# Optimization experiments

Measured on AMD Instinct MI355X. Metric: run time of the kernel, lower is better.

Reference implementation:

```python
import jax, jax.numpy as jnp
import numpy as np

N_EMBDS = 1024
N_HEADS = 16
HEAD_DIM = N_EMBDS // N_HEADS


def setup_inputs() -> dict:
    key = jax.random.key(0)
    ks = jax.random.split(key, 5)
    B, T, C = 2, 2048, N_EMBDS
    x = jax.random.normal(ks[0], (B, T, C), dtype=jnp.float32)
    s = 1.0 / np.sqrt(C)
    W_attn = jax.random.normal(ks[1], (C, 3 * C), dtype=jnp.float32) * s
    b_attn = jnp.zeros((3 * C,), dtype=jnp.float32)
    W_proj = jax.random.normal(ks[2], (C, C), dtype=jnp.float32) * s
    b_proj = jnp.zeros((C,), dtype=jnp.float32)
    return {"x": x, "W_attn": W_attn, "b_attn": b_attn, "W_proj": W_proj, "b_proj": b_proj}


def reference(x, W_attn, b_attn, W_proj, b_proj):
    B, T, C = x.shape
    H, D = N_HEADS, HEAD_DIM
    qkv = x @ W_attn + b_attn  # [B, T, 3C]
    q, k, v = jnp.split(qkv, 3, axis=-1)
    # [B, H, T, D]
    q = q.reshape(B, T, H, D).transpose(0, 2, 1, 3)
    k = k.reshape(B, T, H, D).transpose(0, 2, 1, 3)
    v = v.reshape(B, T, H, D).transpose(0, 2, 1, 3)
    att = jnp.einsum('bhqd,bhkd->bhqk', q, k) * (1.0 / np.sqrt(D))  # [B,H,T,T]
    causal = jnp.tril(jnp.ones((T, T), dtype=bool))
    att = jnp.where(causal[None, None], att, -jnp.inf)
    att = jax.nn.softmax(att, axis=-1)
    y = jnp.einsum('bhqk,bhkd->bhqd', att, v)  # [B,H,T,D]
    y = y.transpose(0, 2, 1, 3).reshape(B, T, C)
    return y @ W_proj + b_proj
```

## Files before the change

kernel.cpp:

```cpp
#include <hip/hip_runtime.h>
#include <hip/hip_bf16.h>


typedef __bf16 bf16x8 __attribute__((ext_vector_type(8)));
typedef float  f32x4  __attribute__((ext_vector_type(4)));
#define BF16 __hip_bfloat16

constexpr int Bb = 2, Tt = 2048, Cc = 1024, Hh = 16, Dd = 64;
constexpr float NEG_INF = -1e30f;

__device__ __forceinline__ f32x4 mfma16(bf16x8 a, bf16x8 b, f32x4 c) {
  return __builtin_amdgcn_mfma_f32_16x16x32_bf16(a, b, c, 0, 0, 0);
}

__device__ __forceinline__ void gll16(const void* g, void* l) {
  __builtin_amdgcn_global_load_lds((const __attribute__((address_space(1))) void*)g,
                                   (__attribute__((address_space(3))) void*)l,
                                   16, 0, 0);
}

__device__ __forceinline__ int swz64(int r, int c) {
  return r * 64 + ((((c >> 3) ^ r) & 7) << 3) + (c & 7);
}

__global__ void cast_kernel(const float* __restrict__ in, BF16* __restrict__ out,
                            int n) {
  const int i = (blockIdx.x * 256 + threadIdx.x) * 8;
  const float4 a = *(const float4*)&in[i];
  const float4 b = *(const float4*)&in[i + 4];
  BF16 o[8];
  o[0] = __float2bfloat16(a.x); o[1] = __float2bfloat16(a.y);
  o[2] = __float2bfloat16(a.z); o[3] = __float2bfloat16(a.w);
  o[4] = __float2bfloat16(b.x); o[5] = __float2bfloat16(b.y);
  o[6] = __float2bfloat16(b.z); o[7] = __float2bfloat16(b.w);
  *(uint4*)&out[i] = *(const uint4*)o;
}

__global__ void transpose_cast(const float* __restrict__ in, BF16* __restrict__ outT,
                               int K, int N) {
  __shared__ float tile[32][33];
  const int n0 = blockIdx.x * 32, k0 = blockIdx.y * 32;
  const int tx = threadIdx.x, ty = threadIdx.y;
#pragma unroll
  for (int i = ty; i < 32; i += 8) tile[i][tx] = in[(size_t)(k0 + i) * N + (n0 + tx)];
  __syncthreads();
#pragma unroll
  for (int i = ty; i < 32; i += 8)
    outT[(size_t)(n0 + i) * K + (k0 + tx)] = __float2bfloat16(tile[tx][i]);
}

__global__ void transpose_v(const BF16* __restrict__ in, BF16* __restrict__ out) {
  __shared__ BF16 tile[32][33];
  const int t0 = blockIdx.x * 32, d0 = blockIdx.y * 32, bh = blockIdx.z;
  const BF16* src = in + (size_t)bh * Tt * Dd;
  BF16* dst = out + (size_t)bh * Tt * Dd;
  const int tx = threadIdx.x, ty = threadIdx.y;
#pragma unroll
  for (int i = ty; i < 32; i += 8) tile[i][tx] = src[(size_t)(t0 + i) * Dd + (d0 + tx)];
  __syncthreads();
#pragma unroll
  for (int i = ty; i < 32; i += 8) dst[(size_t)(d0 + i) * Tt + (t0 + tx)] = tile[tx][i];
}

template <int MODE>
__global__ __launch_bounds__(256) void gemm_bt(const BF16* __restrict__ A,
                                               const BF16* __restrict__ Bt,
                                               const float* __restrict__ bias,
                                               BF16* __restrict__ oq,
                                               BF16* __restrict__ ok,
                                               BF16* __restrict__ ov,
                                               float* __restrict__ fout,
                                               int Ndim, int Kdim) {
  __shared__ alignas(16) BF16 sA[128 * 32];
  __shared__ alignas(16) BF16 sB[128 * 32];
  const int tid = threadIdx.x;
  const int wave = tid >> 6, lane = tid & 63;
  const int quad = lane >> 4, l16 = lane & 15;
  const int wm = (wave >> 1) * 64, wn = (wave & 1) * 64;
  const int bm = blockIdx.y * 128, bn = blockIdx.x * 128;

  f32x4 acc[4][4];
#pragma unroll
  for (int i = 0; i < 4; ++i)
#pragma unroll
    for (int j = 0; j < 4; ++j) acc[i][j] = f32x4{0.f, 0.f, 0.f, 0.f};

  const int rowA = wave * 32 + (lane >> 2);
  const int sub8 = (lane & 3) * 8;
  const BF16* gA0 = &A[(size_t)(bm + rowA) * Kdim + sub8];
  const BF16* gB0 = &Bt[(size_t)(bn + rowA) * Kdim + sub8];
  const size_t rstep16 = (size_t)16 * Kdim;
  BF16* lA0 = &sA[wave * 1024];
  BF16* lA1 = &sA[wave * 1024 + 512];
  BF16* lB0 = &sB[wave * 1024];
  BF16* lB1 = &sB[wave * 1024 + 512];

  for (int k0 = 0; k0 < Kdim; k0 += 32) {
    __syncthreads();
    gll16(gA0 + k0, lA0);
    gll16(gA0 + rstep16 + k0, lA1);
    gll16(gB0 + k0, lB0);
    gll16(gB0 + rstep16 + k0, lB1);
    __syncthreads();

    bf16x8 af[4], bf_[4];
#pragma unroll
    for (int i = 0; i < 4; ++i)
      af[i] = *(const bf16x8*)&sA[(wm + i * 16 + l16) * 32 + quad * 8];
#pragma unroll
    for (int j = 0; j < 4; ++j)
      bf_[j] = *(const bf16x8*)&sB[(wn + j * 16 + l16) * 32 + quad * 8];
#pragma unroll
    for (int i = 0; i < 4; ++i)
#pragma unroll
      for (int j = 0; j < 4; ++j) acc[i][j] = mfma16(af[i], bf_[j], acc[i][j]);
  }

#pragma unroll
  for (int j = 0; j < 4; ++j) {
    const int gn = bn + wn + j * 16 + l16;
    const float bsv = bias[gn];
#pragma unroll
    for (int i = 0; i < 4; ++i) {
#pragma unroll
      for (int r = 0; r < 4; ++r) {
        const int gm = bm + wm + i * 16 + quad * 4 + r;
        float val = acc[i][j][r] + bsv;
        if (MODE == 0) {
          const int which = gn >> 10, c = gn & 1023;
          const int hh = c >> 6, dd = c & 63;
          const int bb = gm >> 11, tk = gm & 2047;
          if (which == 0) val *= 0.125f;
          BF16* dst = (which == 0) ? oq : (which == 1) ? ok : ov;
          dst[(((size_t)(bb * Hh + hh)) * Tt + tk) * Dd + dd] = __float2bfloat16(val);
        } else {
          fout[(size_t)gm * Ndim + gn] = val;
        }
      }
    }
  }
}

__global__ __launch_bounds__(256) void attn_kernel(const BF16* __restrict__ qg,
                                                   const BF16* __restrict__ kg,
                                                   const BF16* __restrict__ vtg,
                                                   BF16* __restrict__ yb) {
  __shared__ alignas(16) BF16 sK[64 * 64];
  __shared__ alignas(16) BF16 sV[64 * 64];
  __shared__ alignas(16) BF16 sP[4][16 * 64];
  const int pr = blockIdx.x, h = blockIdx.y, b = blockIdx.z;
  const int qtA = pr, qtB = 31 - pr;
  const int tid = threadIdx.x;
  const int wave = tid >> 6, lane = tid & 63;
  const int quad = lane >> 4, l16 = lane & 15;
  const size_t base = ((size_t)(b * Hh + h)) * Tt * Dd;

  bf16x8 qA0, qA1, qB0, qB1;
  {
    const size_t offA = base + (size_t)(qtA * 64 + wave * 16 + l16) * Dd;
    const size_t offB = base + (size_t)(qtB * 64 + wave * 16 + l16) * Dd;
    qA0 = *(const bf16x8*)&qg[offA + quad * 8];
    qA1 = *(const bf16x8*)&qg[offA + 32 + quad * 8];
    qB0 = *(const bf16x8*)&qg[offB + quad * 8];
    qB1 = *(const bf16x8*)&qg[offB + 32 + quad * 8];
  }

  bf16x8 vones;
#pragma unroll
  for (int j = 0; j < 8; ++j) vones[j] = (__bf16)1.0f;

  f32x4 oA[4], oB[4], oLA, oLB;
#pragma unroll
  for (int i = 0; i < 4; ++i) {
    oA[i] = f32x4{0.f, 0.f, 0.f, 0.f};
    oB[i] = f32x4{0.f, 0.f, 0.f, 0.f};
  }
  oLA = f32x4{0.f, 0.f, 0.f, 0.f};
  oLB = f32x4{0.f, 0.f, 0.f, 0.f};

  const int krow = tid >> 2, kcg = (tid & 3) * 16;
  BF16* pw = &sP[wave][0];

  auto process = [&](int jt, int qt, bf16x8 qf0, bf16x8 qf1, f32x4 (&o)[4],
                     f32x4& oL) {
    const int kb = jt * 64;
    f32x4 s4[4];
#pragma unroll
    for (int t = 0; t < 4; ++t) s4[t] = f32x4{0.f, 0.f, 0.f, 0.f};
#pragma unroll
    for (int t = 0; t < 4; ++t) {
      const bf16x8 kf0 = *(const bf16x8*)&sK[swz64(t * 16 + l16, quad * 8)];
      const bf16x8 kf1 = *(const bf16x8*)&sK[swz64(t * 16 + l16, 32 + quad * 8)];
      s4[t] = mfma16(qf0, kf0, s4[t]);
      s4[t] = mfma16(qf1, kf1, s4[t]);
    }

    if (jt == qt) {
      const int qrow = qt * 64 + wave * 16 + quad * 4;
#pragma unroll
      for (int t = 0; t < 4; ++t)
#pragma unroll
        for (int r = 0; r < 4; ++r)
          if (kb + t * 16 + l16 > qrow + r) s4[t][r] = NEG_INF;
    }

#pragma unroll
    for (int t = 0; t < 4; ++t)
#pragma unroll
      for (int r = 0; r < 4; ++r) s4[t][r] = __expf(s4[t][r] - 12.0f);

    asm volatile("s_waitcnt lgkmcnt(0)" ::: "memory");
#pragma unroll
    for (int t = 0; t < 4; ++t)
#pragma unroll
      for (int r = 0; r < 4; ++r)
        pw[swz64(quad * 4 + r, t * 16 + l16)] = __float2bfloat16(s4[t][r]);
    asm volatile("s_waitcnt lgkmcnt(0)" ::: "memory");

#pragma unroll
    for (int c = 0; c < 2; ++c) {
      const bf16x8 pa = *(const bf16x8*)&pw[swz64(l16, c * 32 + quad * 8)];
#pragma unroll
      for (int dt = 0; dt < 4; ++dt) {
        const bf16x8 vb = *(const bf16x8*)&sV[swz64(dt * 16 + l16, c * 32 + quad * 8)];
        o[dt] = mfma16(pa, vb, o[dt]);
      }
      oL = mfma16(pa, vones, oL);
    }
  };

  for (int jt = 0; jt <= qtB; ++jt) {
    const int kb = jt * 64;
    __syncthreads();
    {
      const uint4* pk = (const uint4*)&kg[base + (size_t)(kb + krow) * Dd + kcg];
      const uint4* pv = (const uint4*)&vtg[base + (size_t)krow * Tt + kb + kcg];
      uint4 k0 = pk[0], k1 = pk[1];
      uint4 v0 = pv[0], v1 = pv[1];
      *(uint4*)&sK[swz64(krow, kcg)]     = k0;
      *(uint4*)&sK[swz64(krow, kcg + 8)] = k1;
      *(uint4*)&sV[swz64(krow, kcg)]     = v0;
      *(uint4*)&sV[swz64(krow, kcg + 8)] = v1;
    }
    __syncthreads();

    if (jt <= qtA) process(jt, qtA, qA0, qA1, oA, oLA);
    process(jt, qtB, qB0, qB1, oB, oLB);
  }

  auto epi = [&](int qt, f32x4 (&o)[4], f32x4& oL) {
#pragma unroll
    for (int r = 0; r < 4; ++r) {
      const float inv = 1.0f / oL[r];
      const int trow = qt * 64 + wave * 16 + quad * 4 + r;
#pragma unroll
      for (int dt = 0; dt < 4; ++dt)
        yb[((size_t)(b * Tt + trow)) * Cc + h * Dd + dt * 16 + l16] =
            __float2bfloat16(o[dt][r] * inv);
    }
  };
  epi(qtA, oA, oLA);
  epi(qtB, oB, oLB);
}

extern "C" void kernel_launch(void* const* d_in, const int* in_sizes, int n_in,
                              void* d_out, int out_size, void* d_ws, size_t ws_size,
                              hipStream_t stream) {
  (void)in_sizes; (void)n_in; (void)out_size; (void)ws_size;
  const float* x      = (const float*)d_in[0];
  const float* W_attn = (const float*)d_in[1];
  const float* b_attn = (const float*)d_in[2];
  const float* W_proj = (const float*)d_in[3];
  const float* b_proj = (const float*)d_in[4];
  float* out = (float*)d_out;

  constexpr size_t SZ_WA = (size_t)3072 * 1024;
  constexpr size_t SZ_WP = (size_t)1024 * 1024;
  constexpr size_t SZ_X  = (size_t)4096 * 1024;
  constexpr size_t SZ_T  = (size_t)Bb * Hh * Tt * Dd;

  BF16* ws   = (BF16*)d_ws;
  BF16* wtAb = ws;
  BF16* wtPb = wtAb + SZ_WA;
  BF16* xb   = wtPb + SZ_WP;
  BF16* q    = xb + SZ_X;
  BF16* k    = q + SZ_T;
  BF16* v    = k + SZ_T;
  BF16* vt   = v + SZ_T;
  BF16* yb   = vt + SZ_T;

  cast_kernel<<<dim3(2048), 256, 0, stream>>>(x, xb, (int)SZ_X);
  transpose_cast<<<dim3(96, 32), dim3(32, 8), 0, stream>>>(W_attn, wtAb, 1024, 3072);
  transpose_cast<<<dim3(32, 32), dim3(32, 8), 0, stream>>>(W_proj, wtPb, 1024, 1024);
  gemm_bt<0><<<dim3(24, 32), 256, 0, stream>>>(xb, wtAb, b_attn, q, k, v, nullptr,
                                               3072, 1024);
  transpose_v<<<dim3(64, 2, 32), dim3(32, 8), 0, stream>>>(v, vt);
  attn_kernel<<<dim3(16, 16, 2), 256, 0, stream>>>(q, k, vt, yb);
  gemm_bt<1><<<dim3(8, 32), 256, 0, stream>>>(yb, wtPb, b_proj, nullptr, nullptr,
                                              nullptr, out, 1024, 1024);
}
```

Baseline: 201.3 us.

## Keep softmax probabilities in registers via transposed S and fuse prep kernels

The attention kernel now computes S transposed (K as the A operand), so each lane's exp'd probabilities already form the A-fragment for a 16x16x16 bf16 MFMA against V. This removes the per-wave shared-memory round trip for P and its waitcnt barriers, and it interleaves the two query tiles so each K/V fragment read is shared by both. The three preprocessing launches (x cast, two weight transposes) are merged into one kernel indexed by block id to cut launch overhead. The trade-off is twice as many smaller-K MFMAs for PV, plus higher register pressure from holding both tiles' score accumulators at once.

```diff
diff --git a/kernel.cpp b/kernel.cpp
--- a/kernel.cpp
+++ b/kernel.cpp
@@ -3,6 +3,8 @@
 
 
 typedef __bf16 bf16x8 __attribute__((ext_vector_type(8)));
+typedef __bf16 bf16x4 __attribute__((ext_vector_type(4)));
+typedef short  short4v __attribute__((ext_vector_type(4)));
 typedef float  f32x4  __attribute__((ext_vector_type(4)));
 #define BF16 __hip_bfloat16
 
@@ -12,6 +14,23 @@
 __device__ __forceinline__ f32x4 mfma16(bf16x8 a, bf16x8 b, f32x4 c) {
   return __builtin_amdgcn_mfma_f32_16x16x32_bf16(a, b, c, 0, 0, 0);
 }
+
+#if __has_builtin(__builtin_amdgcn_mfma_f32_16x16x16bf16_1k)
+__device__ __forceinline__ f32x4 mfma16k(bf16x4 a, bf16x4 b, f32x4 c) {
+  return __builtin_amdgcn_mfma_f32_16x16x16bf16_1k(
+      __builtin_bit_cast(short4v, a), __builtin_bit_cast(short4v, b), c, 0, 0, 0);
+}
+#elif __has_builtin(__builtin_amdgcn_mfma_f32_16x16x16_bf16)
+__device__ __forceinline__ f32x4 mfma16k(bf16x4 a, bf16x4 b, f32x4 c) {
+  return __builtin_amdgcn_mfma_f32_16x16x16_bf16(a, b, c, 0, 0, 0);
+}
+#else
+__device__ __forceinline__ f32x4 mfma16k(bf16x4 a, bf16x4 b, f32x4 c) {
+  asm volatile("v_mfma_f32_16x16x16_bf16 %0, %1, %2, %0"
+               : "+v"(c) : "v"(a), "v"(b));
+  return c;
+}
+#endif
 
 __device__ __forceinline__ void gll16(const void* g, void* l) {
   __builtin_amdgcn_global_load_lds((const __attribute__((address_space(1))) void*)g,
@@ -23,24 +42,33 @@
   return r * 64 + ((((c >> 3) ^ r) & 7) << 3) + (c & 7);
 }
 
-__global__ void cast_kernel(const float* __restrict__ in, BF16* __restrict__ out,
-                            int n) {
-  const int i = (blockIdx.x * 256 + threadIdx.x) * 8;
-  const float4 a = *(const float4*)&in[i];
-  const float4 b = *(const float4*)&in[i + 4];
-  BF16 o[8];
-  o[0] = __float2bfloat16(a.x); o[1] = __float2bfloat16(a.y);
-  o[2] = __float2bfloat16(a.z); o[3] = __float2bfloat16(a.w);
-  o[4] = __float2bfloat16(b.x); o[5] = __float2bfloat16(b.y);
-  o[6] = __float2bfloat16(b.z); o[7] = __float2bfloat16(b.w);
-  *(uint4*)&out[i] = *(const uint4*)o;
-}
-
-__global__ void transpose_cast(const float* __restrict__ in, BF16* __restrict__ outT,
-                               int K, int N) {
+__global__ void prep_kernel(const float* __restrict__ x, BF16* __restrict__ xb,
+                            const float* __restrict__ Wa, BF16* __restrict__ WaT,
+                            const float* __restrict__ Wp, BF16* __restrict__ WpT) {
   __shared__ float tile[32][33];
-  const int n0 = blockIdx.x * 32, k0 = blockIdx.y * 32;
-  const int tx = threadIdx.x, ty = threadIdx.y;
+  const int bx = blockIdx.x, tid = threadIdx.x;
+  if (bx < 2048) {
+    const int i = (bx * 256 + tid) * 8;
+    const float4 a = *(const float4*)&x[i];
+    const float4 b = *(const float4*)&x[i + 4];
+    BF16 o[8];
+    o[0] = __float2bfloat16(a.x); o[1] = __float2bfloat16(a.y);
+    o[2] = __float2bfloat16(a.z); o[3] = __float2bfloat16(a.w);
+    o[4] = __float2bfloat16(b.x); o[5] = __float2bfloat16(b.y);
+    o[6] = __float2bfloat16(b.z); o[7] = __float2bfloat16(b.w);
+    *(uint4*)&xb[i] = *(const uint4*)o;
+    return;
+  }
+  const float* in; BF16* outT; int K, N, gx, gy;
+  if (bx < 5120) {
+    const int idx = bx - 2048;
+    in = Wa; outT = WaT; K = 1024; N = 3072; gx = idx % 96; gy = idx / 96;
+  } else {
+    const int idx = bx - 5120;
+    in = Wp; outT = WpT; K = 1024; N = 1024; gx = idx % 32; gy = idx / 32;
+  }
+  const int n0 = gx * 32, k0 = gy * 32;
+  const int tx = tid & 31, ty = tid >> 5;
 #pragma unroll
   for (int i = ty; i < 32; i += 8) tile[i][tx] = in[(size_t)(k0 + i) * N + (n0 + tx)];
   __syncthreads();
@@ -147,89 +175,36 @@
                                                    BF16* __restrict__ yb) {
   __shared__ alignas(16) BF16 sK[64 * 64];
   __shared__ alignas(16) BF16 sV[64 * 64];
-  __shared__ alignas(16) BF16 sP[4][16 * 64];
   const int pr = blockIdx.x, h = blockIdx.y, b = blockIdx.z;
-  const int qtA = pr, qtB = 31 - pr;
+  const int qt[2] = {pr, 31 - pr};
   const int tid = threadIdx.x;
   const int wave = tid >> 6, lane = tid & 63;
   const int quad = lane >> 4, l16 = lane & 15;
   const size_t base = ((size_t)(b * Hh + h)) * Tt * Dd;
 
-  bf16x8 qA0, qA1, qB0, qB1;
-  {
-    const size_t offA = base + (size_t)(qtA * 64 + wave * 16 + l16) * Dd;
-    const size_t offB = base + (size_t)(qtB * 64 + wave * 16 + l16) * Dd;
-    qA0 = *(const bf16x8*)&qg[offA + quad * 8];
-    qA1 = *(const bf16x8*)&qg[offA + 32 + quad * 8];
-    qB0 = *(const bf16x8*)&qg[offB + quad * 8];
-    qB1 = *(const bf16x8*)&qg[offB + 32 + quad * 8];
-  }
-
-  bf16x8 vones;
-#pragma unroll
-  for (int j = 0; j < 8; ++j) vones[j] = (__bf16)1.0f;
-
-  f32x4 oA[4], oB[4], oLA, oLB;
-#pragma unroll
-  for (int i = 0; i < 4; ++i) {
-    oA[i] = f32x4{0.f, 0.f, 0.f, 0.f};
-    oB[i] = f32x4{0.f, 0.f, 0.f, 0.f};
-  }
-  oLA = f32x4{0.f, 0.f, 0.f, 0.f};
-  oLB = f32x4{0.f, 0.f, 0.f, 0.f};
+  bf16x8 qf[2][2];
+#pragma unroll
+  for (int s = 0; s < 2; ++s) {
+    const size_t off = base + (size_t)(qt[s] * 64 + wave * 16 + l16) * Dd;
+    qf[s][0] = *(const bf16x8*)&qg[off + quad * 8];
+    qf[s][1] = *(const bf16x8*)&qg[off + 32 + quad * 8];
+  }
+
+  bf16x4 ones4;
+#pragma unroll
+  for (int j = 0; j < 4; ++j) ones4[j] = (__bf16)1.0f;
+
+  f32x4 o[2][4], oL[2];
+#pragma unroll
+  for (int s = 0; s < 2; ++s) {
+#pragma unroll
+    for (int i = 0; i < 4; ++i) o[s][i] = f32x4{0.f, 0.f, 0.f, 0.f};
+    oL[s] = f32x4{0.f, 0.f, 0.f, 0.f};
+  }
 
   const int krow = tid >> 2, kcg = (tid & 3) * 16;
-  BF16* pw = &sP[wave][0];
-
-  auto process = [&](int jt, int qt, bf16x8 qf0, bf16x8 qf1, f32x4 (&o)[4],
-                     f32x4& oL) {
-    const int kb = jt * 64;
-    f32x4 s4[4];
-#pragma unroll
-    for (int t = 0; t < 4; ++t) s4[t] = f32x4{0.f, 0.f, 0.f, 0.f};
-#pragma unroll
-    for (int t = 0; t < 4; ++t) {
-      const bf16x8 kf0 = *(const bf16x8*)&sK[swz64(t * 16 + l16, quad * 8)];
-      const bf16x8 kf1 = *(const bf16x8*)&sK[swz64(t * 16 + l16, 32 + quad * 8)];
-      s4[t] = mfma16(qf0, kf0, s4[t]);
-      s4[t] = mfma16(qf1, kf1, s4[t]);
-    }
-
-    if (jt == qt) {
-      const int qrow = qt * 64 + wave * 16 + quad * 4;
-#pragma unroll
-      for (int t = 0; t < 4; ++t)
-#pragma unroll
-        for (int r = 0; r < 4; ++r)
-          if (kb + t * 16 + l16 > qrow + r) s4[t][r] = NEG_INF;
-    }
-
-#pragma unroll
-    for (int t = 0; t < 4; ++t)
-#pragma unroll
-      for (int r = 0; r < 4; ++r) s4[t][r] = __expf(s4[t][r] - 12.0f);
-
-    asm volatile("s_waitcnt lgkmcnt(0)" ::: "memory");
-#pragma unroll
-    for (int t = 0; t < 4; ++t)
-#pragma unroll
-      for (int r = 0; r < 4; ++r)
-        pw[swz64(quad * 4 + r, t * 16 + l16)] = __float2bfloat16(s4[t][r]);
-    asm volatile("s_waitcnt lgkmcnt(0)" ::: "memory");
-
-#pragma unroll
-    for (int c = 0; c < 2; ++c) {
-      const bf16x8 pa = *(const bf16x8*)&pw[swz64(l16, c * 32 + quad * 8)];
-#pragma unroll
-      for (int dt = 0; dt < 4; ++dt) {
-        const bf16x8 vb = *(const bf16x8*)&sV[swz64(dt * 16 + l16, c * 32 + quad * 8)];
-        o[dt] = mfma16(pa, vb, o[dt]);
-      }
-      oL = mfma16(pa, vones, oL);
-    }
-  };
-
-  for (int jt = 0; jt <= qtB; ++jt) {
+
+  for (int jt = 0; jt <= qt[1]; ++jt) {
     const int kb = jt * 64;
     __syncthreads();
     {
@@ -244,23 +219,66 @@
     }
     __syncthreads();
 
-    if (jt <= qtA) process(jt, qtA, qA0, qA1, oA, oLA);
-    process(jt, qtB, qB0, qB1, oB, oLB);
-  }
-
-  auto epi = [&](int qt, f32x4 (&o)[4], f32x4& oL) {
+    const bool actA = (jt <= qt[0]);
+
+    f32x4 sS[2][4];
+#pragma unroll
+    for (int t = 0; t < 4; ++t) {
+      const bf16x8 kf0 = *(const bf16x8*)&sK[swz64(t * 16 + l16, quad * 8)];
+      const bf16x8 kf1 = *(const bf16x8*)&sK[swz64(t * 16 + l16, 32 + quad * 8)];
+      sS[1][t] = mfma16(kf0, qf[1][0], f32x4{0.f, 0.f, 0.f, 0.f});
+      sS[1][t] = mfma16(kf1, qf[1][1], sS[1][t]);
+      if (actA) {
+        sS[0][t] = mfma16(kf0, qf[0][0], f32x4{0.f, 0.f, 0.f, 0.f});
+        sS[0][t] = mfma16(kf1, qf[0][1], sS[0][t]);
+      }
+    }
+
+    bf16x4 pf[2][4];
+#pragma unroll
+    for (int s = 0; s < 2; ++s) {
+      if (s == 0 && !actA) continue;
+      if (jt == qt[s]) {
+        const int q = qt[s] * 64 + wave * 16 + l16;
+#pragma unroll
+        for (int t = 0; t < 4; ++t)
+#pragma unroll
+          for (int r = 0; r < 4; ++r)
+            if (kb + t * 16 + quad * 4 + r > q) sS[s][t][r] = NEG_INF;
+      }
+#pragma unroll
+      for (int t = 0; t < 4; ++t)
+#pragma unroll
+        for (int r = 0; r < 4; ++r)
+          pf[s][t][r] = (__bf16)__expf(sS[s][t][r] - 12.0f);
+    }
+
+#pragma unroll
+    for (int t = 0; t < 4; ++t) {
+#pragma unroll
+      for (int dt = 0; dt < 4; ++dt) {
+        const bf16x4 vb =
+            *(const bf16x4*)&sV[swz64(dt * 16 + l16, t * 16 + quad * 4)];
+        o[1][dt] = mfma16k(pf[1][t], vb, o[1][dt]);
+        if (actA) o[0][dt] = mfma16k(pf[0][t], vb, o[0][dt]);
+      }
+      oL[1] = mfma16k(pf[1][t], ones4, oL[1]);
+      if (actA) oL[0] = mfma16k(pf[0][t], ones4, oL[0]);
+    }
+  }
+
+#pragma unroll
+  for (int s = 0; s < 2; ++s) {
 #pragma unroll
     for (int r = 0; r < 4; ++r) {
-      const float inv = 1.0f / oL[r];
-      const int trow = qt * 64 + wave * 16 + quad * 4 + r;
+      const float inv = 1.0f / oL[s][r];
+      const int trow = qt[s] * 64 + wave * 16 + quad * 4 + r;
 #pragma unroll
       for (int dt = 0; dt < 4; ++dt)
         yb[((size_t)(b * Tt + trow)) * Cc + h * Dd + dt * 16 + l16] =
-            __float2bfloat16(o[dt][r] * inv);
-    }
-  };
-  epi(qtA, oA, oLA);
-  epi(qtB, oB, oLB);
+            __float2bfloat16(o[s][dt][r] * inv);
+    }
+  }
 }
 
 extern "C" void kernel_launch(void* const* d_in, const int* in_sizes, int n_in,
@@ -289,9 +307,7 @@
   BF16* vt   = v + SZ_T;
   BF16* yb   = vt + SZ_T;
 
-  cast_kernel<<<dim3(2048), 256, 0, stream>>>(x, xb, (int)SZ_X);
-  transpose_cast<<<dim3(96, 32), dim3(32, 8), 0, stream>>>(W_attn, wtAb, 1024, 3072);
-  transpose_cast<<<dim3(32, 32), dim3(32, 8), 0, stream>>>(W_proj, wtPb, 1024, 1024);
+  prep_kernel<<<dim3(6144), 256, 0, stream>>>(x, xb, W_attn, wtAb, W_proj, wtPb);
   gemm_bt<0><<<dim3(24, 32), 256, 0, stream>>>(xb, wtAb, b_attn, q, k, v, nullptr,
                                                3072, 1024);
   transpose_v<<<dim3(64, 2, 32), dim3(32, 8), 0, stream>>>(v, vt);
```

New measurement: 210.7 us. 4.7% more time.
